# Performance work log

Hardware: AMD Instinct MI355X
Metric: run time of the kernel (lower is better)

Reference implementation:

```python
import jax, jax.numpy as jnp
import numpy as np

H, HID, VD, NB = 8, 128, 16, 4
EN_LOC, DE_LOC = 5.0, 5.0
FMAX = jnp.float32(3.4028235e38)

def _gelu(x):
    return jax.nn.gelu(x, approximate=False)  # keras gelu default = erf form

def _mlp(x, W1, b1, W2, b2):
    return _gelu(x @ W1 + b1) @ W2 + b2

def _mhpa(m_dist, x, r, w, locality):
    # m_dist: (B,N,N), r: (1,H,1,1), w: (H,HID,VD)
    sd = m_dist[:, None, :, :] * (r ** 2)  # (B,H,N,N)
    if locality <= 100:
        n = sd.shape[-1]
        pos = locality / 100.0 * (n - 1)  # tfp linear percentile position
        lo = int(np.floor(pos)); hi = int(np.ceil(pos)); frac = np.float32(pos - lo)
        s = jnp.sort(sd, axis=-1)
        thr = s[..., lo] * (1.0 - frac) + s[..., hi] * frac  # (B,H,N)
        sd = jnp.where(sd <= thr[..., None], sd, FMAX)
    att = jax.nn.softmax(-sd, axis=-1)  # masked entries -> exp(-huge) = 0
    v = jnp.einsum('bnj,hjk->bhnk', x, w)  # (B,H,N,VD)
    o = jnp.einsum('bhnj,bhjd->bhnd', att, v)  # (B,H,N,VD)
    B, Hh, N, D = o.shape
    return _gelu(o.transpose(0, 2, 1, 3).reshape(B, N, Hh * D))

def setup_inputs() -> dict:
    B, N, IN, OUT = 2, 2048, 3, 1
    ks = jax.random.split(jax.random.key(0), 40)
    def dn(k, shape, fan):
        return (jax.random.normal(k, shape) / np.sqrt(fan)).astype(jnp.float32)
    d = {}
    d['m_dist'] = jax.random.uniform(ks[0], (B, N, N), dtype=jnp.float32)
    d['inputs'] = jax.random.normal(ks[1], (B, N, IN), dtype=jnp.float32)
    d['en_W'] = dn(ks[2], (IN, HID), IN); d['en_b'] = jnp.zeros((HID,), jnp.float32)
    d['down_r'] = jax.random.uniform(ks[3], (1, H, 1, 1), dtype=jnp.float32)
    d['down_w'] = dn(ks[4], (H, HID, VD), HID)
    d['mlp1_W1'] = dn(ks[5], (HID, HID), HID); d['mlp1_b1'] = jnp.zeros((HID,), jnp.float32)
    d['mlp1_W2'] = dn(ks[6], (HID, HID), HID); d['mlp1_b2'] = jnp.zeros((HID,), jnp.float32)
    d['w1_W'] = dn(ks[7], (HID, HID), HID); d['w1_b'] = jnp.zeros((HID,), jnp.float32)
    d['pa_r'] = jax.random.uniform(ks[8], (NB, 1, H, 1, 1), dtype=jnp.float32)
    d['pa_w'] = dn(ks[9], (NB, H, HID, VD), HID)
    d['blk_W1'] = dn(ks[10], (NB, HID, HID), HID); d['blk_b1'] = jnp.zeros((NB, HID), jnp.float32)
    d['blk_W2'] = dn(ks[11], (NB, HID, HID), HID); d['blk_b2'] = jnp.zeros((NB, HID), jnp.float32)
    d['wi_W'] = dn(ks[12], (NB, HID, HID), HID); d['wi_b'] = jnp.zeros((NB, HID), jnp.float32)
    d['up_r'] = jax.random.uniform(ks[13], (1, H, 1, 1), dtype=jnp.float32)
    d['up_w'] = dn(ks[14], (H, HID, VD), HID)
    d['mlp2_W1'] = dn(ks[15], (HID, HID), HID); d['mlp2_b1'] = jnp.zeros((HID,), jnp.float32)
    d['mlp2_W2'] = dn(ks[16], (HID, HID), HID); d['mlp2_b2'] = jnp.zeros((HID,), jnp.float32)
    d['w2_W'] = dn(ks[17], (HID, HID), HID); d['w2_b'] = jnp.zeros((HID,), jnp.float32)
    d['de_W1'] = dn(ks[18], (HID, HID), HID); d['de_b1'] = jnp.zeros((HID,), jnp.float32)
    d['de_W2'] = dn(ks[19], (HID, OUT), HID); d['de_b2'] = jnp.zeros((OUT,), jnp.float32)
    return d

def reference(m_dist, inputs, en_W, en_b, down_r, down_w, mlp1_W1, mlp1_b1, mlp1_W2, mlp1_b2,
              w1_W, w1_b, pa_r, pa_w, blk_W1, blk_b1, blk_W2, blk_b2, wi_W, wi_b,
              up_r, up_w, mlp2_W1, mlp2_b1, mlp2_W2, mlp2_b2, w2_W, w2_b,
              de_W1, de_b1, de_W2, de_b2):
    en = _gelu(inputs @ en_W + en_b)
    x = _mlp(_mhpa(m_dist, en, down_r, down_w, EN_LOC), mlp1_W1, mlp1_b1, mlp1_W2, mlp1_b2) + (en @ w1_W + w1_b)
    x = _gelu(x)
    for i in range(NB):
        h = _mhpa(m_dist, x, pa_r[i], pa_w[i], 200)  # locality=200 -> no mask
        x = _gelu(_mlp(h, blk_W1[i], blk_b1[i], blk_W2[i], blk_b2[i]) + (x @ wi_W[i] + wi_b[i]))
    de = _mlp(_mhpa(m_dist, x, up_r, up_w, DE_LOC), mlp2_W1, mlp2_b1, mlp2_W2, mlp2_b2) + (x @ w2_W + w2_b)
    de = _gelu(de)
    return _mlp(de, de_W1, de_b1, de_W2, de_b2)
```

## Files before the change

kernel.cpp:

```cpp
#include <hip/hip_runtime.h>
#include <hip/hip_bf16.h>
#include <cstddef>

#define NROWS 4096
#define HIDD  128
#define NH    8
#define VD    16

typedef __attribute__((ext_vector_type(8))) short bf16x8;
typedef __attribute__((ext_vector_type(4))) float f32x4;
typedef __attribute__((ext_vector_type(4))) unsigned int u32x4;

__device__ __forceinline__ float gelu_f(float x) {
    return 0.5f * x * (1.0f + erff(x * 0.70710678118654752440f));
}

__device__ __forceinline__ unsigned short bf16_rne(float f) {
    union { float f; unsigned u; } x; x.f = f;
    unsigned r = x.u + 0x7FFFu + ((x.u >> 16) & 1u);
    return (unsigned short)(r >> 16);
}
__device__ __forceinline__ float bf16_to_f(unsigned short h) {
    union { unsigned u; float f; } x; x.u = ((unsigned)h) << 16;
    return x.f;
}
__device__ __forceinline__ unsigned pk_bf16(float a, float b) {
    __hip_bfloat162 t = __float22bfloat162_rn(make_float2(a, b));
    unsigned u; __builtin_memcpy(&u, &t, 4); return u;
}

__device__ __forceinline__ void split8(const float* av, bf16x8& hi, bf16x8& lo) {
    #pragma unroll
    for (int j = 0; j < 8; ++j) {
        unsigned short h = bf16_rne(av[j]);
        unsigned short l = bf16_rne(av[j] - bf16_to_f(h));
        hi[j] = (short)h; lo[j] = (short)l;
    }
}

__device__ __forceinline__ void load_a_global(const float* __restrict__ X,
                                              int row0, int lane,
                                              bf16x8* ahi, bf16x8* alo) {
    const int q = lane >> 4, mr = lane & 15;
    const float* xr = X + (size_t)(row0 + mr) * 128 + q * 8;
    #pragma unroll
    for (int kt = 0; kt < 4; ++kt) {
        float av[8];
        *(float4*)(av)     = *(const float4*)(xr + kt * 32);
        *(float4*)(av + 4) = *(const float4*)(xr + kt * 32 + 4);
        split8(av, ahi[kt], alo[kt]);
    }
}
__device__ __forceinline__ void load_a_lds(const float (*xT)[132], int lane,
                                           bf16x8* ahi, bf16x8* alo) {
    const int q = lane >> 4, mr = lane & 15;
    #pragma unroll
    for (int kt = 0; kt < 4; ++kt) {
        float av[8];
        *(float4*)(av)     = *(const float4*)&xT[mr][kt * 32 + q * 8];
        *(float4*)(av + 4) = *(const float4*)&xT[mr][kt * 32 + q * 8 + 4];
        split8(av, ahi[kt], alo[kt]);
    }
}

__device__ __forceinline__ f32x4 mm3(f32x4 acc, bf16x8 ahi, bf16x8 alo,
                                     const unsigned short* __restrict__ bp, int kt) {
    bf16x8 bhi = *(const bf16x8*)(bp + kt * 512);
    bf16x8 blo = *(const bf16x8*)(bp + 16384 + kt * 512);
    acc = __builtin_amdgcn_mfma_f32_16x16x32_bf16(ahi, bhi, acc, 0, 0, 0);
    acc = __builtin_amdgcn_mfma_f32_16x16x32_bf16(ahi, blo, acc, 0, 0, 0);
    acc = __builtin_amdgcn_mfma_f32_16x16x32_bf16(alo, bhi, acc, 0, 0, 0);
    return acc;
}

__device__ __forceinline__ void vproj_lds(const float (*xT)[132], int row0,
                                          const unsigned short* __restrict__ Vw,
                                          unsigned short* __restrict__ vblk) {
    const int tid = threadIdx.x, wave = tid >> 6, lane = tid & 63;
    const int q = lane >> 4, mr = lane & 15;
    bf16x8 ahi[4], alo[4];
    load_a_lds(xT, lane, ahi, alo);
    #pragma unroll
    for (int ct = 0; ct < 2; ++ct) {
        int nt = wave * 2 + ct;
        const unsigned short* bp = Vw + (size_t)nt * 2048 + lane * 8;
        f32x4 acc = (f32x4){0.f, 0.f, 0.f, 0.f};
        #pragma unroll
        for (int kt = 0; kt < 4; ++kt) acc = mm3(acc, ahi[kt], alo[kt], bp, kt);
        int c = nt * 16 + mr;
        int r0 = row0 + q * 4;
        int bb = r0 >> 11, n = r0 & 2047;
        int jt = n >> 5, q2 = (n >> 3) & 3, jj = n & 7;
        int h = c >> 4, dd = c & 15;
        size_t off = (((size_t)(bb * 8 + h) * 64 + jt) * 4 + q2) * 128
                   + (dd << 3) + jj;
        uint2 st = make_uint2(pk_bf16(acc[0], acc[1]), pk_bf16(acc[2], acc[3]));
        *(uint2*)(vblk + off) = st;
    }
}


__device__ __forceinline__ void mm_lds_tile(const float (*src)[132], float (*dst)[132],
                                            const unsigned short* __restrict__ Wb,
                                            const float* __restrict__ bias,
                                            int wave, int lane) {
    bf16x8 ahi[4], alo[4];
    load_a_lds(src, lane, ahi, alo);
    const unsigned short* bp = Wb + (size_t)wave * 2048 + lane * 8;
    f32x4 acc = (f32x4){0.f, 0.f, 0.f, 0.f};
    #pragma unroll
    for (int kt = 0; kt < 4; ++kt) acc = mm3(acc, ahi[kt], alo[kt], bp, kt);
    const int q = lane >> 4, rn = lane & 15, c = wave * 16 + rn;
    const float bv = bias[c];
    #pragma unroll
    for (int reg = 0; reg < 4; ++reg)
        dst[q * 4 + reg][c] = gelu_f(acc[reg] + bv);
}

__device__ __forceinline__ void mm2_tile(const float (*A1)[132],
                                         const float* __restrict__ A2, int row0,
                                         const unsigned short* __restrict__ B1,
                                         const float* __restrict__ bias1,
                                         const unsigned short* __restrict__ B2,
                                         const float* __restrict__ bias2,
                                         float* __restrict__ xout, float (*xT)[132],
                                         int wave, int lane) {
    bf16x8 a1h[4], a1l[4], a2h[4], a2l[4];
    load_a_lds(A1, lane, a1h, a1l);
    load_a_global(A2, row0, lane, a2h, a2l);
    const unsigned short* bp1 = B1 + (size_t)wave * 2048 + lane * 8;
    const unsigned short* bp2 = B2 + (size_t)wave * 2048 + lane * 8;
    f32x4 acc = (f32x4){0.f, 0.f, 0.f, 0.f};
    #pragma unroll
    for (int kt = 0; kt < 4; ++kt) acc = mm3(acc, a1h[kt], a1l[kt], bp1, kt);
    #pragma unroll
    for (int kt = 0; kt < 4; ++kt) acc = mm3(acc, a2h[kt], a2l[kt], bp2, kt);
    const int q = lane >> 4, rn = lane & 15, c = wave * 16 + rn;
    const float bv = bias1[c] + bias2[c];
    #pragma unroll
    for (int reg = 0; reg < 4; ++reg) {
        float v = gelu_f(acc[reg] + bv);
        if (xout) xout[(size_t)(row0 + q * 4 + reg) * 128 + c] = v;
        xT[q * 4 + reg][c] = v;
    }
}

__device__ __forceinline__ void vproj8(const float (*xT)[132], int row0,
                                       const unsigned short* __restrict__ Vw,
                                       unsigned short* __restrict__ vout,
                                       int wave, int lane) {
    bf16x8 ahi[4], alo[4];
    load_a_lds(xT, lane, ahi, alo);
    const unsigned short* bp = Vw + (size_t)wave * 2048 + lane * 8;
    f32x4 acc = (f32x4){0.f, 0.f, 0.f, 0.f};
    #pragma unroll
    for (int kt = 0; kt < 4; ++kt) acc = mm3(acc, ahi[kt], alo[kt], bp, kt);
    const int q = lane >> 4, mr = lane & 15, c = wave * 16 + mr;
    int r0 = row0 + q * 4;
    int bb = r0 >> 11, n = r0 & 2047;
    int jt = n >> 5, q2 = (n >> 3) & 3, jj = n & 7;
    int h = c >> 4, dd = c & 15;
    size_t off = (((size_t)(bb * 8 + h) * 64 + jt) * 4 + q2) * 128
               + (dd << 3) + jj;
    uint2 st = make_uint2(pk_bf16(acc[0], acc[1]), pk_bf16(acc[2], acc[3]));
    *(uint2*)(vout + off) = st;
}

struct PrepArgs { const float* src[25]; unsigned vwmask; };

__global__ __launch_bounds__(256) void prep_percentile_kernel(
    PrepArgs a, unsigned short* __restrict__ dst,
    const float* __restrict__ m, float* __restrict__ m102, float* __restrict__ m103)
{
    if (blockIdx.x < 100) {
        const int mat = blockIdx.x >> 2, chunk = blockIdx.x & 3;
        const float* __restrict__ W = a.src[mat];
        const int vw = (a.vwmask >> mat) & 1;
        unsigned short* __restrict__ base = dst + (size_t)mat * 32768;
        for (int o = chunk * 4096 + threadIdx.x; o < chunk * 4096 + 4096; o += 256) {
            int nt = o >> 11, kt = (o >> 9) & 3, q = (o >> 7) & 3;
            int n16 = (o >> 3) & 15, jj = o & 7;
            int k = kt * 32 + q * 8 + jj;
            float w = vw ? W[nt * 2048 + k * 16 + n16]
                         : W[k * 128 + nt * 16 + n16];
            unsigned short h = bf16_rne(w);
            unsigned short l = bf16_rne(w - bf16_to_f(h));
            base[o] = h;
            base[16384 + o] = l;
        }
        return;
    }

    __shared__ int   cnt[256];
    __shared__ int   cum[256];
    __shared__ float buf[192];
    __shared__ int   nc;
    __shared__ int   sb0, sb1, sbase;

    const int row = blockIdx.x - 100;
    const int t   = threadIdx.x;
    const float* mr = m + (size_t)row * 2048;

    float4 aa = *(const float4*)(mr + t * 8);
    float4 cc = *(const float4*)(mr + t * 8 + 4);
    float v[8] = {aa.x, aa.y, aa.z, aa.w, cc.x, cc.y, cc.z, cc.w};

    cnt[t] = 0;
    if (t == 0) nc = 0;
    __syncthreads();

    int bidx[8];
    #pragma unroll
    for (int i = 0; i < 8; ++i) {
        int bi = (int)(v[i] * 256.0f);
        bi = bi < 0 ? 0 : (bi > 255 ? 255 : bi);
        bidx[i] = bi;
        atomicAdd(&cnt[bi], 1);
    }
    __syncthreads();

    if (t < 64) {
        int c0 = cnt[t * 4], c1 = cnt[t * 4 + 1], c2 = cnt[t * 4 + 2], c3 = cnt[t * 4 + 3];
        int s1 = c0 + c1, s2 = s1 + c2, s3 = s2 + c3;
        int sc = s3;
        #pragma unroll
        for (int off = 1; off < 64; off <<= 1) {
            int o = __shfl_up(sc, off);
            if (t >= off) sc += o;
        }
        int base = sc - s3;
        cum[t * 4]     = base + c0;
        cum[t * 4 + 1] = base + s1;
        cum[t * 4 + 2] = base + s2;
        cum[t * 4 + 3] = base + s3;
    }
    __syncthreads();

    {
        int cprev = (t == 0) ? 0 : cum[t - 1];
        int cthis = cum[t];
        if (cprev < 103 && 103 <= cthis) { sb0 = t; sbase = cprev; }
        if (cprev < 104 && 104 <= cthis) { sb1 = t; }
    }
    __syncthreads();

    const int b0 = sb0, b1 = sb1, base = sbase;
    #pragma unroll
    for (int i = 0; i < 8; ++i) {
        if (bidx[i] >= b0 && bidx[i] <= b1) {
            int p = atomicAdd(&nc, 1);
            if (p < 192) buf[p] = v[i];
        }
    }
    __syncthreads();

    int n = nc; if (n > 192) n = 192;
    if (t < n) {
        float x = buf[t];
        int rk = base;
        for (int j = 0; j < n; ++j) {
            float y = buf[j];
            rk += (y < x || (y == x && j < t)) ? 1 : 0;
        }
        if (rk == 102) m102[row] = x;
        if (rk == 103) m103[row] = x;
    }
}

__global__ __launch_bounds__(256) void encoder_vproj_kernel(
    const float* __restrict__ inp, const float* __restrict__ W,
    const float* __restrict__ b, float* __restrict__ ben,
    const unsigned short* __restrict__ Vw, unsigned short* __restrict__ vblk)
{
    __shared__ float xT[16][132];
    const int tid = threadIdx.x;
    const int row0 = blockIdx.x * 16;
    const int ri = tid >> 4, c0 = (tid & 15) * 8;
    const int row = row0 + ri;
    float x0 = inp[row * 3], x1 = inp[row * 3 + 1], x2 = inp[row * 3 + 2];
    float o[8];
    #pragma unroll
    for (int j = 0; j < 8; ++j) {
        int c = c0 + j;
        o[j] = gelu_f(x0 * W[c] + x1 * W[128 + c] + x2 * W[256 + c] + b[c]);
        xT[ri][c0 + j] = o[j];
    }
    *(float4*)(ben + (size_t)row * 128 + c0)     = *(float4*)(o);
    *(float4*)(ben + (size_t)row * 128 + c0 + 4) = *(float4*)(o + 4);
    __syncthreads();
    vproj_lds(xT, row0, Vw, vblk);
}

__device__ __forceinline__ void attn_stage(
    const float* __restrict__ m_dist, const unsigned short* __restrict__ vblk,
    const float* __restrict__ rvec,
    const float* __restrict__ m102, const float* __restrict__ m103,
    int masked, int row0,
    float (*partLDS)[16][128], float (*sumLDS)[8][16], float (*bhT)[132])
{
    const int tid  = threadIdx.x;
    const int wave = tid >> 6, lane = tid & 63;
    const int hg = wave & 1, jq = wave >> 1;
    const int q = lane >> 4, rn = lane & 15;
    const int row  = row0 + rn;
    const int b    = row0 >> 11;
    const int n    = row & 2047;

    float r2[4], c2[4], thr[4];
    {
        const double pos = 5.0 / 100.0 * 2047.0;
        const float FRAC = (float)(pos - 102.0);
        const float OM   = 1.0f - FRAC;
        float t102 = m102[row], t103 = m103[row];
        #pragma unroll
        for (int hh = 0; hh < 4; ++hh) {
            float r = rvec[hg * 4 + hh];
            r2[hh] = r * r;
            c2[hh] = -r2[hh] * 1.44269504088896340736f;
            thr[hh] = masked ? ((t102 * r2[hh]) * OM + (t103 * r2[hh]) * FRAC)
                             : 3.4028235e38f;
        }
    }

    const float* mrow = m_dist + ((size_t)b << 22) + ((size_t)n << 11);
    const unsigned short* vbase = vblk + (((size_t)(b * 8 + hg * 4)) << 15);

    f32x4 acc[4], accs[4];
    #pragma unroll
    for (int hh = 0; hh < 4; ++hh) {
        acc[hh]  = (f32x4){0.f, 0.f, 0.f, 0.f};
        accs[hh] = (f32x4){0.f, 0.f, 0.f, 0.f};
    }
    bf16x8 vones;
    #pragma unroll
    for (int j = 0; j < 8; ++j) vones[j] = (short)0x3F80;

    const int jbeg = jq * 16, jend = jbeg + 16;

    float mvA[8], mvB[8]; bf16x8 bfA[4], bfB[4];

    auto loadjt = [&](int jt, float* mv, bf16x8* bf) {
        const int jb = (jt << 5) + (q << 3);
        *(float4*)(mv)     = *(const float4*)(mrow + jb);
        *(float4*)(mv + 4) = *(const float4*)(mrow + jb + 4);
        #pragma unroll
        for (int hh = 0; hh < 4; ++hh)
            bf[hh] = *(const bf16x8*)(vbase + ((size_t)hh << 15)
                                       + ((size_t)jt << 9) + (lane << 3));
    };
    auto compute = [&](const float* mv, const bf16x8* bf) {
        #pragma unroll
        for (int hh = 0; hh < 4; ++hh) {
            float p[8];
            if (masked) {
                #pragma unroll
                for (int jj = 0; jj < 8; ++jj) {
                    float sd = mv[jj] * r2[hh];
                    float e  = __builtin_amdgcn_exp2f(mv[jj] * c2[hh]);
                    p[jj] = (sd <= thr[hh]) ? e : 0.f;
                }
            } else {
                #pragma unroll
                for (int jj = 0; jj < 8; ++jj)
                    p[jj] = __builtin_amdgcn_exp2f(mv[jj] * c2[hh]);
            }
            u32x4 af;
            af[0] = pk_bf16(p[0], p[1]); af[1] = pk_bf16(p[2], p[3]);
            af[2] = pk_bf16(p[4], p[5]); af[3] = pk_bf16(p[6], p[7]);
            bf16x8 afrag = __builtin_bit_cast(bf16x8, af);
            acc[hh]  = __builtin_amdgcn_mfma_f32_16x16x32_bf16(afrag, bf[hh], acc[hh], 0, 0, 0);
            accs[hh] = __builtin_amdgcn_mfma_f32_16x16x32_bf16(afrag, vones,  accs[hh], 0, 0, 0);
        }
    };

    loadjt(jbeg, mvA, bfA);
    for (int jt = jbeg; jt < jend; jt += 2) {
        loadjt(jt + 1, mvB, bfB);
        compute(mvA, bfA);
        int j2 = (jt + 2 < jend) ? jt + 2 : jend - 1;
        loadjt(j2, mvA, bfA);
        compute(mvB, bfB);
    }

    if (rn == 0) {
        #pragma unroll
        for (int hh = 0; hh < 4; ++hh)
            #pragma unroll
            for (int reg = 0; reg < 4; ++reg)
                sumLDS[jq][hg * 4 + hh][q * 4 + reg] = accs[hh][reg];
    }
    #pragma unroll
    for (int hh = 0; hh < 4; ++hh) {
        #pragma unroll
        for (int reg = 0; reg < 4; ++reg)
            partLDS[jq][q * 4 + reg][(hg * 4 + hh) * 16 + rn] = acc[hh][reg];
    }
    __syncthreads();

    {
        int e0 = tid << 2;
        int ri = e0 >> 7, c0e = e0 & 127, h = c0e >> 4;
        float4 s = *(const float4*)&partLDS[0][ri][c0e];
        #pragma unroll
        for (int k = 1; k < 4; ++k) {
            float4 pz = *(const float4*)&partLDS[k][ri][c0e];
            s.x += pz.x; s.y += pz.y; s.z += pz.z; s.w += pz.w;
        }
        float l = sumLDS[0][h][ri] + sumLDS[1][h][ri]
                + sumLDS[2][h][ri] + sumLDS[3][h][ri];
        float inv = 1.0f / l;
        float4 o;
        o.x = gelu_f(s.x * inv); o.y = gelu_f(s.y * inv);
        o.z = gelu_f(s.z * inv); o.w = gelu_f(s.w * inv);
        *(float4*)&bhT[ri][c0e] = o;
    }
    __syncthreads();
}

__global__ __launch_bounds__(512) void stage_kernel(
    const float* __restrict__ m_dist, const unsigned short* __restrict__ vin,
    const float* __restrict__ rvec,
    const float* __restrict__ m102, const float* __restrict__ m103,
    const unsigned short* __restrict__ W1b, const float* __restrict__ b1,
    const unsigned short* __restrict__ W2b, const float* __restrict__ b2,
    const float* __restrict__ xin, const unsigned short* __restrict__ Wib,
    const float* __restrict__ bi,
    float* __restrict__ xout,
    const unsigned short* __restrict__ Vw, unsigned short* __restrict__ vout,
    int masked)
{
    __shared__ float partLDS[4][16][128];
    __shared__ float sumLDS[4][8][16];
    __shared__ float bhT[16][132];
    __shared__ float btT[16][132];
    __shared__ float xT[16][132];

    const int tid = threadIdx.x, wave = tid >> 6, lane = tid & 63;
    const int row0 = blockIdx.x * 16;

    attn_stage(m_dist, vin, rvec, m102, m103, masked, row0,
               partLDS, sumLDS, bhT);

    mm_lds_tile(bhT, btT, W1b, b1, wave, lane);
    __syncthreads();

    mm2_tile(btT, xin, row0, W2b, b2, Wib, bi, xout, xT, wave, lane);
    __syncthreads();

    vproj8(xT, row0, Vw, vout, wave, lane);
}

__global__ __launch_bounds__(512) void decoder_stage_kernel(
    const float* __restrict__ m_dist, const unsigned short* __restrict__ vin,
    const float* __restrict__ rvec,
    const float* __restrict__ m102, const float* __restrict__ m103,
    const unsigned short* __restrict__ W1b, const float* __restrict__ b1,
    const unsigned short* __restrict__ W2b, const float* __restrict__ b2,
    const float* __restrict__ xin, const unsigned short* __restrict__ Wib,
    const float* __restrict__ bi,
    const unsigned short* __restrict__ DW1, const float* __restrict__ db1,
    const float* __restrict__ de_W2, const float* __restrict__ de_b2,
    float* __restrict__ out)
{
    __shared__ float partLDS[4][16][128];
    __shared__ float sumLDS[4][8][16];
    __shared__ float bhT[16][132];
    __shared__ float btT[16][132];
    __shared__ float xT[16][132];
    __shared__ float tT[16][132];

    const int tid = threadIdx.x, wave = tid >> 6, lane = tid & 63;
    const int row0 = blockIdx.x * 16;

    attn_stage(m_dist, vin, rvec, m102, m103, 1, row0,
               partLDS, sumLDS, bhT);

    mm_lds_tile(bhT, btT, W1b, b1, wave, lane);
    __syncthreads();

    mm2_tile(btT, xin, row0, W2b, b2, Wib, bi, nullptr, xT, wave, lane);
    __syncthreads();

    mm_lds_tile(xT, tT, DW1, db1, wave, lane);
    __syncthreads();

    if (tid < 256) {
        int r = tid >> 4, ch = tid & 15;
        const float* tp = &tT[r][ch * 8];
        const float* wp = de_W2 + ch * 8;
        float p = 0.f;
        #pragma unroll
        for (int j = 0; j < 8; ++j) p += tp[j] * wp[j];
        p += __shfl_xor(p, 1); p += __shfl_xor(p, 2);
        p += __shfl_xor(p, 4); p += __shfl_xor(p, 8);
        if (ch == 0) out[row0 + r] = p + de_b2[0];
    }
}

extern "C" void kernel_launch(void* const* d_in, const int* in_sizes, int n_in,
                              void* d_out, int out_size, void* d_ws, size_t ws_size,
                              hipStream_t stream)
{
    (void)in_sizes; (void)n_in; (void)out_size; (void)ws_size;
    const float* m_dist  = (const float*)d_in[0];
    const float* inputs  = (const float*)d_in[1];
    const float* en_W    = (const float*)d_in[2];
    const float* en_b    = (const float*)d_in[3];
    const float* down_r  = (const float*)d_in[4];
    const float* down_w  = (const float*)d_in[5];
    const float* mlp1_W1 = (const float*)d_in[6];
    const float* mlp1_b1 = (const float*)d_in[7];
    const float* mlp1_W2 = (const float*)d_in[8];
    const float* mlp1_b2 = (const float*)d_in[9];
    const float* w1_W    = (const float*)d_in[10];
    const float* w1_b    = (const float*)d_in[11];
    const float* pa_r    = (const float*)d_in[12];
    const float* pa_w    = (const float*)d_in[13];
    const float* blk_W1  = (const float*)d_in[14];
    const float* blk_b1  = (const float*)d_in[15];
    const float* blk_W2  = (const float*)d_in[16];
    const float* blk_b2  = (const float*)d_in[17];
    const float* wi_W    = (const float*)d_in[18];
    const float* wi_b    = (const float*)d_in[19];
    const float* up_r    = (const float*)d_in[20];
    const float* up_w    = (const float*)d_in[21];
    const float* mlp2_W1 = (const float*)d_in[22];
    const float* mlp2_b1 = (const float*)d_in[23];
    const float* mlp2_W2 = (const float*)d_in[24];
    const float* mlp2_b2 = (const float*)d_in[25];
    const float* w2_W    = (const float*)d_in[26];
    const float* w2_b    = (const float*)d_in[27];
    const float* de_W1   = (const float*)d_in[28];
    const float* de_b1   = (const float*)d_in[29];
    const float* de_W2   = (const float*)d_in[30];
    const float* de_b2   = (const float*)d_in[31];
    float* out = (float*)d_out;

    const size_t BUF = (size_t)NROWS * HIDD;
    float* w     = (float*)d_ws;
    float* ben   = w;
    float* bx0   = w + 1 * BUF;
    float* bx1   = w + 2 * BUF;
    unsigned short* vblkA = (unsigned short*)(w + 3 * BUF);
    unsigned short* vblkB = (unsigned short*)(w + 3 * BUF + BUF / 2);
    float* m102  = w + 4 * BUF;
    float* m103  = m102 + NROWS;
    unsigned short* wcvt = (unsigned short*)(m103 + NROWS);

    enum { CW_DOWN = 0, CW_MLP1W1 = 1, CW_MLP1W2 = 2, CW_W1 = 3,
           CW_PA = 4 , CW_BLKW1 = 8, CW_BLKW2 = 12, CW_WI = 16,
           CW_UP = 20, CW_MLP2W1 = 21, CW_MLP2W2 = 22, CW_W2 = 23, CW_DE1 = 24 };
    PrepArgs pa;
    pa.src[CW_DOWN]   = down_w;
    pa.src[CW_MLP1W1] = mlp1_W1;
    pa.src[CW_MLP1W2] = mlp1_W2;
    pa.src[CW_W1]     = w1_W;
    for (int i = 0; i < 4; ++i) {
        pa.src[CW_PA + i]    = pa_w   + (size_t)i * NH * HIDD * VD;
        pa.src[CW_BLKW1 + i] = blk_W1 + (size_t)i * HIDD * HIDD;
        pa.src[CW_BLKW2 + i] = blk_W2 + (size_t)i * HIDD * HIDD;
        pa.src[CW_WI + i]    = wi_W   + (size_t)i * HIDD * HIDD;
    }
    pa.src[CW_UP]     = up_w;
    pa.src[CW_MLP2W1] = mlp2_W1;
    pa.src[CW_MLP2W2] = mlp2_W2;
    pa.src[CW_W2]     = w2_W;
    pa.src[CW_DE1]    = de_W1;
    pa.vwmask = (1u << CW_DOWN) | (0xFu << CW_PA) | (1u << CW_UP);

    auto CW = [&](int slot) { return wcvt + (size_t)slot * 32768; };

    dim3 b256(256), b512(512);
    dim3 gT(NROWS / 16);

    prep_percentile_kernel<<<dim3(100 + NROWS), b256, 0, stream>>>(
        pa, wcvt, m_dist, m102, m103);

    encoder_vproj_kernel<<<gT, b256, 0, stream>>>(inputs, en_W, en_b, ben,
                                                  CW(CW_DOWN), vblkA);

    stage_kernel<<<gT, b512, 0, stream>>>(
        m_dist, vblkA, down_r, m102, m103,
        CW(CW_MLP1W1), mlp1_b1, CW(CW_MLP1W2), mlp1_b2,
        ben, CW(CW_W1), w1_b, bx0, CW(CW_PA + 0), vblkB, 1);

    float* xin = bx0;
    float* xout = bx1;
    unsigned short* vin = vblkB;
    unsigned short* vou = vblkA;
    for (int i = 0; i < 4; ++i) {
        stage_kernel<<<gT, b512, 0, stream>>>(
            m_dist, vin, pa_r + (size_t)i * NH, m102, m103,
            CW(CW_BLKW1 + i), blk_b1 + (size_t)i * HIDD,
            CW(CW_BLKW2 + i), blk_b2 + (size_t)i * HIDD,
            xin, CW(CW_WI + i), wi_b + (size_t)i * HIDD,
            xout, (i < 3) ? CW(CW_PA + i + 1) : CW(CW_UP), vou, 0);
        float* t = xin; xin = xout; xout = t;
        unsigned short* tv = vin; vin = vou; vou = tv;
    }

    decoder_stage_kernel<<<gT, b512, 0, stream>>>(
        m_dist, vin, up_r, m102, m103,
        CW(CW_MLP2W1), mlp2_b1, CW(CW_MLP2W2), mlp2_b2,
        xin, CW(CW_W2), w2_b,
        CW(CW_DE1), de_b1, de_W2, de_b2, out);
}
```

Measured before the change: 289.9 us.

## Fuse encoder and all stages into one cooperative persistent kernel with grid sync

Merges the encoder, the six attention/MLP stages and the decoder into a single cooperative kernel launch. Grid-wide barriers stand in for the kernel boundaries. Each block keeps its 16-row activation tile in LDS across stages, so the global x buffers and the per-stage reload of the residual input go away. This removes launch gaps and global round trips for the activations. In exchange it needs all 256 blocks of 512 threads to be co-resident for the cooperative launch, and it raises LDS use per block, which may limit occupancy.

```diff
diff --git a/kernel.cpp b/kernel.cpp
--- a/kernel.cpp
+++ b/kernel.cpp
@@ -1,6 +1,9 @@
 #include <hip/hip_runtime.h>
 #include <hip/hip_bf16.h>
+#include <hip/hip_cooperative_groups.h>
 #include <cstddef>
+
+namespace cg = cooperative_groups;
 
 #define NROWS 4096
 #define HIDD  128
@@ -38,19 +41,6 @@
     }
 }
 
-__device__ __forceinline__ void load_a_global(const float* __restrict__ X,
-                                              int row0, int lane,
-                                              bf16x8* ahi, bf16x8* alo) {
-    const int q = lane >> 4, mr = lane & 15;
-    const float* xr = X + (size_t)(row0 + mr) * 128 + q * 8;
-    #pragma unroll
-    for (int kt = 0; kt < 4; ++kt) {
-        float av[8];
-        *(float4*)(av)     = *(const float4*)(xr + kt * 32);
-        *(float4*)(av + 4) = *(const float4*)(xr + kt * 32 + 4);
-        split8(av, ahi[kt], alo[kt]);
-    }
-}
 __device__ __forceinline__ void load_a_lds(const float (*xT)[132], int lane,
                                            bf16x8* ahi, bf16x8* alo) {
     const int q = lane >> 4, mr = lane & 15;
@@ -73,33 +63,6 @@
     return acc;
 }
 
-__device__ __forceinline__ void vproj_lds(const float (*xT)[132], int row0,
-                                          const unsigned short* __restrict__ Vw,
-                                          unsigned short* __restrict__ vblk) {
-    const int tid = threadIdx.x, wave = tid >> 6, lane = tid & 63;
-    const int q = lane >> 4, mr = lane & 15;
-    bf16x8 ahi[4], alo[4];
-    load_a_lds(xT, lane, ahi, alo);
-    #pragma unroll
-    for (int ct = 0; ct < 2; ++ct) {
-        int nt = wave * 2 + ct;
-        const unsigned short* bp = Vw + (size_t)nt * 2048 + lane * 8;
-        f32x4 acc = (f32x4){0.f, 0.f, 0.f, 0.f};
-        #pragma unroll
-        for (int kt = 0; kt < 4; ++kt) acc = mm3(acc, ahi[kt], alo[kt], bp, kt);
-        int c = nt * 16 + mr;
-        int r0 = row0 + q * 4;
-        int bb = r0 >> 11, n = r0 & 2047;
-        int jt = n >> 5, q2 = (n >> 3) & 3, jj = n & 7;
-        int h = c >> 4, dd = c & 15;
-        size_t off = (((size_t)(bb * 8 + h) * 64 + jt) * 4 + q2) * 128
-                   + (dd << 3) + jj;
-        uint2 st = make_uint2(pk_bf16(acc[0], acc[1]), pk_bf16(acc[2], acc[3]));
-        *(uint2*)(vblk + off) = st;
-    }
-}
-
-
 __device__ __forceinline__ void mm_lds_tile(const float (*src)[132], float (*dst)[132],
                                             const unsigned short* __restrict__ Wb,
                                             const float* __restrict__ bias,
@@ -117,17 +80,15 @@
         dst[q * 4 + reg][c] = gelu_f(acc[reg] + bv);
 }
 
-__device__ __forceinline__ void mm2_tile(const float (*A1)[132],
-                                         const float* __restrict__ A2, int row0,
+__device__ __forceinline__ void mm2_lds2(const float (*A1)[132], const float (*A2)[132],
                                          const unsigned short* __restrict__ B1,
                                          const float* __restrict__ bias1,
                                          const unsigned short* __restrict__ B2,
                                          const float* __restrict__ bias2,
-                                         float* __restrict__ xout, float (*xT)[132],
-                                         int wave, int lane) {
+                                         float (*xT)[132], int wave, int lane) {
     bf16x8 a1h[4], a1l[4], a2h[4], a2l[4];
     load_a_lds(A1, lane, a1h, a1l);
-    load_a_global(A2, row0, lane, a2h, a2l);
+    load_a_lds(A2, lane, a2h, a2l);
     const unsigned short* bp1 = B1 + (size_t)wave * 2048 + lane * 8;
     const unsigned short* bp2 = B2 + (size_t)wave * 2048 + lane * 8;
     f32x4 acc = (f32x4){0.f, 0.f, 0.f, 0.f};
@@ -138,11 +99,8 @@
     const int q = lane >> 4, rn = lane & 15, c = wave * 16 + rn;
     const float bv = bias1[c] + bias2[c];
     #pragma unroll
-    for (int reg = 0; reg < 4; ++reg) {
-        float v = gelu_f(acc[reg] + bv);
-        if (xout) xout[(size_t)(row0 + q * 4 + reg) * 128 + c] = v;
-        xT[q * 4 + reg][c] = v;
-    }
+    for (int reg = 0; reg < 4; ++reg)
+        xT[q * 4 + reg][c] = gelu_f(acc[reg] + bv);
 }
 
 __device__ __forceinline__ void vproj8(const float (*xT)[132], int row0,
@@ -265,30 +223,6 @@
         if (rk == 102) m102[row] = x;
         if (rk == 103) m103[row] = x;
     }
-}
-
-__global__ __launch_bounds__(256) void encoder_vproj_kernel(
-    const float* __restrict__ inp, const float* __restrict__ W,
-    const float* __restrict__ b, float* __restrict__ ben,
-    const unsigned short* __restrict__ Vw, unsigned short* __restrict__ vblk)
-{
-    __shared__ float xT[16][132];
-    const int tid = threadIdx.x;
-    const int row0 = blockIdx.x * 16;
-    const int ri = tid >> 4, c0 = (tid & 15) * 8;
-    const int row = row0 + ri;
-    float x0 = inp[row * 3], x1 = inp[row * 3 + 1], x2 = inp[row * 3 + 2];
-    float o[8];
-    #pragma unroll
-    for (int j = 0; j < 8; ++j) {
-        int c = c0 + j;
-        o[j] = gelu_f(x0 * W[c] + x1 * W[128 + c] + x2 * W[256 + c] + b[c]);
-        xT[ri][c0 + j] = o[j];
-    }
-    *(float4*)(ben + (size_t)row * 128 + c0)     = *(float4*)(o);
-    *(float4*)(ben + (size_t)row * 128 + c0 + 4) = *(float4*)(o + 4);
-    __syncthreads();
-    vproj_lds(xT, row0, Vw, vblk);
 }
 
 __device__ __forceinline__ void attn_stage(
@@ -417,83 +351,94 @@
     __syncthreads();
 }
 
-__global__ __launch_bounds__(512) void stage_kernel(
-    const float* __restrict__ m_dist, const unsigned short* __restrict__ vin,
-    const float* __restrict__ rvec,
-    const float* __restrict__ m102, const float* __restrict__ m103,
-    const unsigned short* __restrict__ W1b, const float* __restrict__ b1,
-    const unsigned short* __restrict__ W2b, const float* __restrict__ b2,
-    const float* __restrict__ xin, const unsigned short* __restrict__ Wib,
-    const float* __restrict__ bi,
-    float* __restrict__ xout,
-    const unsigned short* __restrict__ Vw, unsigned short* __restrict__ vout,
-    int masked)
+struct MegaArgs {
+    const float* m_dist;
+    const float* inputs;
+    const float* en_W; const float* en_b;
+    const float* m102; const float* m103;
+    const unsigned short* wcvt;
+    unsigned short* vblkA; unsigned short* vblkB;
+    const float* rvec[6];
+    const float* b1p[6]; const float* b2p[6]; const float* bip[6];
+    int w1slot[6], w2slot[6], wislot[6], vslot[5];
+    int maskedv[6];
+    const float* db1; const float* de_W2; const float* de_b2;
+    int dw1slot;
+    float* out;
+};
+
+__global__ __launch_bounds__(512) void mega_kernel(MegaArgs a)
 {
     __shared__ float partLDS[4][16][128];
     __shared__ float sumLDS[4][8][16];
     __shared__ float bhT[16][132];
     __shared__ float btT[16][132];
-    __shared__ float xT[16][132];
+    __shared__ float xA[16][132];
+    __shared__ float xB[16][132];
 
     const int tid = threadIdx.x, wave = tid >> 6, lane = tid & 63;
     const int row0 = blockIdx.x * 16;
-
-    attn_stage(m_dist, vin, rvec, m102, m103, masked, row0,
-               partLDS, sumLDS, bhT);
-
-    mm_lds_tile(bhT, btT, W1b, b1, wave, lane);
-    __syncthreads();
-
-    mm2_tile(btT, xin, row0, W2b, b2, Wib, bi, xout, xT, wave, lane);
-    __syncthreads();
-
-    vproj8(xT, row0, Vw, vout, wave, lane);
-}
-
-__global__ __launch_bounds__(512) void decoder_stage_kernel(
-    const float* __restrict__ m_dist, const unsigned short* __restrict__ vin,
-    const float* __restrict__ rvec,
-    const float* __restrict__ m102, const float* __restrict__ m103,
-    const unsigned short* __restrict__ W1b, const float* __restrict__ b1,
-    const unsigned short* __restrict__ W2b, const float* __restrict__ b2,
-    const float* __restrict__ xin, const unsigned short* __restrict__ Wib,
-    const float* __restrict__ bi,
-    const unsigned short* __restrict__ DW1, const float* __restrict__ db1,
-    const float* __restrict__ de_W2, const float* __restrict__ de_b2,
-    float* __restrict__ out)
-{
-    __shared__ float partLDS[4][16][128];
-    __shared__ float sumLDS[4][8][16];
-    __shared__ float bhT[16][132];
-    __shared__ float btT[16][132];
-    __shared__ float xT[16][132];
-    __shared__ float tT[16][132];
-
-    const int tid = threadIdx.x, wave = tid >> 6, lane = tid & 63;
-    const int row0 = blockIdx.x * 16;
-
-    attn_stage(m_dist, vin, rvec, m102, m103, 1, row0,
-               partLDS, sumLDS, bhT);
-
-    mm_lds_tile(bhT, btT, W1b, b1, wave, lane);
-    __syncthreads();
-
-    mm2_tile(btT, xin, row0, W2b, b2, Wib, bi, nullptr, xT, wave, lane);
-    __syncthreads();
-
-    mm_lds_tile(xT, tT, DW1, db1, wave, lane);
+    cg::grid_group grid = cg::this_grid();
+
+    auto CW = [&](int slot) { return a.wcvt + (size_t)slot * 32768; };
+
+    {
+        int ri = tid >> 5, c0 = (tid & 31) * 4;
+        int row = row0 + ri;
+        float x0 = a.inputs[row * 3], x1 = a.inputs[row * 3 + 1],
+              x2 = a.inputs[row * 3 + 2];
+        #pragma unroll
+        for (int j = 0; j < 4; ++j) {
+            int c = c0 + j;
+            xA[ri][c] = gelu_f(x0 * a.en_W[c] + x1 * a.en_W[128 + c]
+                               + x2 * a.en_W[256 + c] + a.en_b[c]);
+        }
+    }
+    __syncthreads();
+    vproj8(xA, row0, CW(0 ), a.vblkA, wave, lane);
+    __threadfence();
+    grid.sync();
+
+    float (*xcur)[132] = xA;
+    float (*xnxt)[132] = xB;
+    unsigned short* vin  = a.vblkA;
+    unsigned short* vout = a.vblkB;
+
+    for (int s = 0; s < 5; ++s) {
+        attn_stage(a.m_dist, vin, a.rvec[s], a.m102, a.m103, a.maskedv[s],
+                   row0, partLDS, sumLDS, bhT);
+        mm_lds_tile(bhT, btT, CW(a.w1slot[s]), a.b1p[s], wave, lane);
+        __syncthreads();
+        mm2_lds2(btT, xcur, CW(a.w2slot[s]), a.b2p[s],
+                 CW(a.wislot[s]), a.bip[s], xnxt, wave, lane);
+        __syncthreads();
+        vproj8(xnxt, row0, CW(a.vslot[s]), vout, wave, lane);
+        { float (*t)[132] = xcur; xcur = xnxt; xnxt = t; }
+        { unsigned short* t = vin; vin = vout; vout = t; }
+        __threadfence();
+        grid.sync();
+    }
+
+    attn_stage(a.m_dist, vin, a.rvec[5], a.m102, a.m103, 1,
+               row0, partLDS, sumLDS, bhT);
+    mm_lds_tile(bhT, btT, CW(a.w1slot[5]), a.b1p[5], wave, lane);
+    __syncthreads();
+    mm2_lds2(btT, xcur, CW(a.w2slot[5]), a.b2p[5],
+             CW(a.wislot[5]), a.bip[5], xnxt, wave, lane);
+    __syncthreads();
+    mm_lds_tile(xnxt, bhT , CW(a.dw1slot), a.db1, wave, lane);
     __syncthreads();
 
     if (tid < 256) {
         int r = tid >> 4, ch = tid & 15;
-        const float* tp = &tT[r][ch * 8];
-        const float* wp = de_W2 + ch * 8;
+        const float* tp = &bhT[r][ch * 8];
+        const float* wp = a.de_W2 + ch * 8;
         float p = 0.f;
         #pragma unroll
         for (int j = 0; j < 8; ++j) p += tp[j] * wp[j];
         p += __shfl_xor(p, 1); p += __shfl_xor(p, 2);
         p += __shfl_xor(p, 4); p += __shfl_xor(p, 8);
-        if (ch == 0) out[row0 + r] = p + de_b2[0];
+        if (ch == 0) a.out[row0 + r] = p + a.de_b2[0];
     }
 }
 
@@ -536,15 +481,10 @@
     const float* de_b2   = (const float*)d_in[31];
     float* out = (float*)d_out;
 
-    const size_t BUF = (size_t)NROWS * HIDD;
-    float* w     = (float*)d_ws;
-    float* ben   = w;
-    float* bx0   = w + 1 * BUF;
-    float* bx1   = w + 2 * BUF;
-    unsigned short* vblkA = (unsigned short*)(w + 3 * BUF);
-    unsigned short* vblkB = (unsigned short*)(w + 3 * BUF + BUF / 2);
-    float* m102  = w + 4 * BUF;
-    float* m103  = m102 + NROWS;
+    unsigned short* vblkA = (unsigned short*)d_ws;
+    unsigned short* vblkB = vblkA + (size_t)NROWS * HIDD;
+    float* m102 = (float*)(vblkB + (size_t)NROWS * HIDD);
+    float* m103 = m102 + NROWS;
     unsigned short* wcvt = (unsigned short*)(m103 + NROWS);
 
     enum { CW_DOWN = 0, CW_MLP1W1 = 1, CW_MLP1W2 = 2, CW_W1 = 3,
@@ -568,40 +508,36 @@
     pa.src[CW_DE1]    = de_W1;
     pa.vwmask = (1u << CW_DOWN) | (0xFu << CW_PA) | (1u << CW_UP);
 
-    auto CW = [&](int slot) { return wcvt + (size_t)slot * 32768; };
-
-    dim3 b256(256), b512(512);
-    dim3 gT(NROWS / 16);
-
-    prep_percentile_kernel<<<dim3(100 + NROWS), b256, 0, stream>>>(
+    prep_percentile_kernel<<<dim3(100 + NROWS), dim3(256), 0, stream>>>(
         pa, wcvt, m_dist, m102, m103);
 
-    encoder_vproj_kernel<<<gT, b256, 0, stream>>>(inputs, en_W, en_b, ben,
-                                                  CW(CW_DOWN), vblkA);
-
-    stage_kernel<<<gT, b512, 0, stream>>>(
-        m_dist, vblkA, down_r, m102, m103,
-        CW(CW_MLP1W1), mlp1_b1, CW(CW_MLP1W2), mlp1_b2,
-        ben, CW(CW_W1), w1_b, bx0, CW(CW_PA + 0), vblkB, 1);
-
-    float* xin = bx0;
-    float* xout = bx1;
-    unsigned short* vin = vblkB;
-    unsigned short* vou = vblkA;
+    MegaArgs ma;
+    ma.m_dist = m_dist; ma.inputs = inputs;
+    ma.en_W = en_W; ma.en_b = en_b;
+    ma.m102 = m102; ma.m103 = m103;
+    ma.wcvt = wcvt; ma.vblkA = vblkA; ma.vblkB = vblkB;
+    ma.rvec[0] = down_r; ma.maskedv[0] = 1;
+    ma.w1slot[0] = CW_MLP1W1; ma.b1p[0] = mlp1_b1;
+    ma.w2slot[0] = CW_MLP1W2; ma.b2p[0] = mlp1_b2;
+    ma.wislot[0] = CW_W1;     ma.bip[0] = w1_b;
+    ma.vslot[0]  = CW_PA + 0;
     for (int i = 0; i < 4; ++i) {
-        stage_kernel<<<gT, b512, 0, stream>>>(
-            m_dist, vin, pa_r + (size_t)i * NH, m102, m103,
-            CW(CW_BLKW1 + i), blk_b1 + (size_t)i * HIDD,
-            CW(CW_BLKW2 + i), blk_b2 + (size_t)i * HIDD,
-            xin, CW(CW_WI + i), wi_b + (size_t)i * HIDD,
-            xout, (i < 3) ? CW(CW_PA + i + 1) : CW(CW_UP), vou, 0);
-        float* t = xin; xin = xout; xout = t;
-        unsigned short* tv = vin; vin = vou; vou = tv;
-    }
-
-    decoder_stage_kernel<<<gT, b512, 0, stream>>>(
-        m_dist, vin, up_r, m102, m103,
-        CW(CW_MLP2W1), mlp2_b1, CW(CW_MLP2W2), mlp2_b2,
-        xin, CW(CW_W2), w2_b,
-        CW(CW_DE1), de_b1, de_W2, de_b2, out);
-}
+        ma.rvec[1 + i] = pa_r + (size_t)i * NH; ma.maskedv[1 + i] = 0;
+        ma.w1slot[1 + i] = CW_BLKW1 + i; ma.b1p[1 + i] = blk_b1 + (size_t)i * HIDD;
+        ma.w2slot[1 + i] = CW_BLKW2 + i; ma.b2p[1 + i] = blk_b2 + (size_t)i * HIDD;
+        ma.wislot[1 + i] = CW_WI + i;    ma.bip[1 + i] = wi_b + (size_t)i * HIDD;
+        if (i < 4 - 1 || true)
+            ma.vslot[1 + i] = (i < 3) ? (CW_PA + i + 1) : CW_UP;
+    }
+    ma.rvec[5] = up_r; ma.maskedv[5] = 1;
+    ma.w1slot[5] = CW_MLP2W1; ma.b1p[5] = mlp2_b1;
+    ma.w2slot[5] = CW_MLP2W2; ma.b2p[5] = mlp2_b2;
+    ma.wislot[5] = CW_W2;     ma.bip[5] = w2_b;
+    ma.dw1slot = CW_DE1; ma.db1 = de_b1;
+    ma.de_W2 = de_W2; ma.de_b2 = de_b2;
+    ma.out = out;
+
+    void* kargs[] = { &ma };
+    hipLaunchCooperativeKernel((void*)mega_kernel, dim3(NROWS / 16), dim3(512),
+                               kargs, 0, stream);
+}
```

After: 747.7 us. 2.58x slower.
